# Optimization experiments

Hardware: AMD Instinct MI355X
Metric: run time of the kernel (lower is better)

The kernel has to match this reference:

```python
import jax, jax.numpy as jnp
import numpy as np

N, E = 50000, 800000
IN_DIM, H, OUT = 16, 256, 64
L = 3
REL_DIM, ROLE_DIM, COL_DIM = 16, 8, 8
NUM_REL, NUM_ROLE, NUM_COL = 8, 8, 3
EDGE_IN = 2 * H + REL_DIM + 2 * ROLE_DIM + 2 * COL_DIM   # 560
NODE_IN = 2 * H + ROLE_DIM + COL_DIM                     # 528
LN_EPS = 1e-5


def setup_inputs() -> dict:
    key = jax.random.key(0)
    ks = jax.random.split(key, 32)
    s = 0.02
    inp = {
        "scalars": jax.random.normal(ks[0], (N, IN_DIM), jnp.float32),
        "edge_index": jax.random.randint(ks[1], (2, E), 0, N),
        "edge_relation": jax.random.randint(ks[2], (E,), 0, NUM_REL),
        "node_color_rep": jax.random.randint(ks[3], (N,), 0, NUM_COL),
        "node_role": jax.random.randint(ks[4], (N,), 0, NUM_ROLE),
        # block-level embeddings + input projection (weights stored [in,out])
        "blk_role_emb": jax.random.normal(ks[5], (NUM_ROLE, 8), jnp.float32) * s,
        "blk_color_emb": jax.random.normal(ks[6], (NUM_COL, 8), jnp.float32) * s,
        "in_w": jax.random.normal(ks[7], (IN_DIM + 16, H), jnp.float32) * s,
        "in_b": jnp.zeros((H,), jnp.float32),
        # per-layer params, stacked over L
        "rel_embs": jax.random.normal(ks[8], (L, NUM_REL, REL_DIM), jnp.float32) * s,
        "role_embs": jax.random.normal(ks[9], (L, NUM_ROLE, ROLE_DIM), jnp.float32) * s,
        "col_embs": jax.random.normal(ks[10], (L, NUM_COL, COL_DIM), jnp.float32) * s,
        "e1_w": jax.random.normal(ks[11], (L, EDGE_IN, H), jnp.float32) * s,
        "e1_b": jnp.zeros((L, H), jnp.float32),
        "e2_w": jax.random.normal(ks[12], (L, H, H), jnp.float32) * s,
        "e2_b": jnp.zeros((L, H), jnp.float32),
        "n1_w": jax.random.normal(ks[13], (L, NODE_IN, H), jnp.float32) * s,
        "n1_b": jnp.zeros((L, H), jnp.float32),
        "n2_w": jax.random.normal(ks[14], (L, H, H), jnp.float32) * s,
        "n2_b": jnp.zeros((L, H), jnp.float32),
        "ln_g": jnp.ones((L, H), jnp.float32),
        "ln_b": jnp.zeros((L, H), jnp.float32),
        "out_w": jax.random.normal(ks[15], (H, OUT), jnp.float32) * s,
        "out_b": jnp.zeros((OUT,), jnp.float32),
    }
    return inp


def _layer(h, edge_index, edge_relation, node_color_rep, node_role,
           rel_e, role_e, col_e, e1w, e1b, e2w, e2b, n1w, n1b, n2w, n2b, g, b):
    src, dst = edge_index[0], edge_index[1]
    role_all = role_e[node_role]           # [N, ROLE_DIM]
    col_all = col_e[node_color_rep]        # [N, COL_DIM]
    edge_in = jnp.concatenate(
        [h[src], h[dst], rel_e[edge_relation],
         role_all[src], role_all[dst], col_all[src], col_all[dst]], axis=-1)
    m = jax.nn.silu(edge_in @ e1w + e1b)
    m = jax.nn.silu(m @ e2w + e2b)                       # [E, H]
    agg = jax.ops.segment_sum(m, dst, num_segments=h.shape[0])
    node_in = jnp.concatenate([h, agg, role_all, col_all], axis=-1)
    upd = jax.nn.silu(node_in @ n1w + n1b) @ n2w + n2b
    x = h + upd
    mu = jnp.mean(x, axis=-1, keepdims=True)
    var = jnp.mean(jnp.square(x - mu), axis=-1, keepdims=True)
    return g * (x - mu) * jax.lax.rsqrt(var + LN_EPS) + b


def reference(scalars, edge_index, edge_relation, node_color_rep, node_role,
              blk_role_emb, blk_color_emb, in_w, in_b,
              rel_embs, role_embs, col_embs,
              e1_w, e1_b, e2_w, e2_b, n1_w, n1_b, n2_w, n2_b,
              ln_g, ln_b, out_w, out_b):
    node_in = jnp.concatenate(
        [scalars, blk_color_emb[node_color_rep], blk_role_emb[node_role]], axis=-1)
    h = node_in @ in_w + in_b
    for i in range(L):
        h = _layer(h, edge_index, edge_relation, node_color_rep, node_role,
                   rel_embs[i], role_embs[i], col_embs[i],
                   e1_w[i], e1_b[i], e2_w[i], e2_b[i],
                   n1_w[i], n1_b[i], n2_w[i], n2_b[i],
                   ln_g[i], ln_b[i])
    return h @ out_w + out_b
```

## Files before the change

kernel.cpp:

```cpp
#include <hip/hip_runtime.h>

#define NN 50000
#define NE 800000
#define H 256
#define NB 12500
#define NBINS 50176
#define HBLK 782

typedef __bf16 bf16x8 __attribute__((ext_vector_type(8)));
typedef __bf16 bf16x4 __attribute__((ext_vector_type(4)));
typedef float f32x4 __attribute__((ext_vector_type(4)));

static __device__ __forceinline__ f32x4 mfma16(bf16x8 a, bf16x8 b, f32x4 c) {
  return __builtin_amdgcn_mfma_f32_16x16x32_bf16(a, b, c, 0, 0, 0);
}
static __device__ __forceinline__ bf16x8 bzero8() {
  bf16x8 z;
#pragma unroll
  for (int j = 0; j < 8; ++j) z[j] = (__bf16)0.f;
  return z;
}
static __device__ __forceinline__ float silu_f(float v) {
  return v * __builtin_amdgcn_rcpf(1.f + __builtin_amdgcn_exp2f(v * -1.442695041f));
}

__global__ void preph_kernel(
    const float* __restrict__ e1w, const float* __restrict__ e2w,
    const float* __restrict__ n1w, const float* __restrict__ n2w,
    const float* __restrict__ outw, const float* __restrict__ e1b,
    const float* __restrict__ n1b,
    const float* __restrict__ rel_embs, const float* __restrict__ role_embs,
    const float* __restrict__ col_embs, const int* __restrict__ dstI,
    __bf16* __restrict__ wsd, __bf16* __restrict__ e2p,
    __bf16* __restrict__ n1p, __bf16* __restrict__ n2p,
    __bf16* __restrict__ outp, int* __restrict__ cnt,
    float* __restrict__ TR, __bf16* __restrict__ TNp,
    __bf16* __restrict__ TSp, __bf16* __restrict__ TDp)
{
  if (blockIdx.x >= 4675) {
    const int e = (blockIdx.x - 4675) * 256 + threadIdx.x;
    if (e < NE) atomicAdd(&cnt[dstI[e]], 1);
    return;
  }
  int i = blockIdx.x * 256 + threadIdx.x;
  if (i < 3 * 131072) {
    const int l = i / 131072, rem = i % 131072;
    const int c = rem >> 14, r2 = rem & 16383;
    const int n = r2 >> 5, k = c * 32 + (r2 & 31);
    wsd[i] = (n < 256) ? (__bf16)e1w[((size_t)l * 560 + k) * 256 + n]
                       : (__bf16)e1w[((size_t)l * 560 + 256 + k) * 256 + (n - 256)];
    return;
  }
  i -= 3 * 131072;
  if (i < 3 * 65536) {
    const int l = i / 65536, rem = i % 65536;
    const int c = rem >> 13, r2 = rem & 8191;
    const int n = r2 >> 5, k = c * 32 + (r2 & 31);
    e2p[i] = (__bf16)e2w[((size_t)l * 256 + k) * 256 + n];
    return;
  }
  i -= 3 * 65536;
  if (i < 3 * 131072) {
    const int l = i / 131072, rem = i % 131072;
    const int c = rem >> 13, r2 = rem & 8191;
    const int n = r2 >> 5, k = c * 32 + (r2 & 31);
    n1p[i] = (__bf16)n1w[((size_t)l * 528 + k) * 256 + n];
    return;
  }
  i -= 3 * 131072;
  if (i < 3 * 65536) {
    const int l = i / 65536, rem = i % 65536;
    const int c = rem >> 13, r2 = rem & 8191;
    const int n = r2 >> 5, k = c * 32 + (r2 & 31);
    n2p[i] = (__bf16)n2w[((size_t)l * 256 + k) * 256 + n];
    return;
  }
  i -= 3 * 65536;
  if (i < 16384) {
    const int c = i >> 11, r2 = i & 2047;
    const int n = r2 >> 5, k = c * 32 + (r2 & 31);
    outp[i] = (__bf16)outw[(size_t)k * 64 + n];
    return;
  }
  i -= 16384;
  if (i < 768) {
    const int l = i >> 8, c = i & 255;
    float w[48];
#pragma unroll
    for (int j = 0; j < 48; ++j) w[j] = e1w[((size_t)l * 560 + 512 + j) * 256 + c];
#pragma unroll
    for (int r = 0; r < 8; ++r) {
      float s = 0.f;
#pragma unroll
      for (int j = 0; j < 16; ++j) s += rel_embs[l * 128 + r * 16 + j] * w[j];
      TR[((size_t)l * 8 + r) * 256 + c] = s;
    }
    float wn[16];
#pragma unroll
    for (int j = 0; j < 16; ++j) wn[j] = n1w[((size_t)l * 528 + 512 + j) * 256 + c];
    const float bias = e1b[l * 256 + c];
    const float nbias = n1b[l * 256 + c];
    const size_t ob = ((size_t)l * 256 + c) * 32;
#pragma unroll
    for (int ro = 0; ro < 8; ++ro) {
      float ss = 0.f, sd = 0.f, sn = 0.f;
#pragma unroll
      for (int j = 0; j < 8; ++j) {
        const float re = role_embs[l * 64 + ro * 8 + j];
        ss += re * w[16 + j];
        sd += re * w[24 + j];
        sn += re * wn[j];
      }
#pragma unroll
      for (int co = 0; co < 3; ++co) {
        float cs = 0.f, cd = 0.f, cn = 0.f;
#pragma unroll
        for (int j = 0; j < 8; ++j) {
          const float ce = col_embs[l * 24 + co * 8 + j];
          cs += ce * w[32 + j];
          cd += ce * w[40 + j];
          cn += ce * wn[8 + j];
        }
        const int k = ro * 3 + co;
        TSp[ob + k] = (__bf16)(ss + cs);
        TDp[ob + k] = (__bf16)(sd + cd + bias);
        TNp[ob + k] = (__bf16)(sn + cn + nbias);
      }
    }
#pragma unroll
    for (int k = 24; k < 32; ++k) {
      TSp[ob + k] = (__bf16)0.f;
      TDp[ob + k] = (__bf16)0.f;
      TNp[ob + k] = (__bf16)0.f;
    }
  }
}

__global__ __launch_bounds__(1024) void scan_kernel(int* __restrict__ cnt,
                                                    int* __restrict__ cnt2) {
  __shared__ int wsum[16];
  __shared__ int carry;
  const int tid = threadIdx.x, lane = tid & 63, wid = tid >> 6;
  if (tid == 0) carry = 0;
  __syncthreads();
  for (int base = 0; base < NBINS; base += 4096) {
    const int idx = base + tid * 4;
    int4 v = make_int4(0, 0, 0, 0);
    if (idx < NBINS) v = *(const int4*)&cnt[idx];
    const int s1 = v.x + v.y, s2 = s1 + v.z, tot = s2 + v.w;
    int x = tot;
#pragma unroll
    for (int d = 1; d < 64; d <<= 1) {
      const int y = __shfl_up(x, d, 64);
      if (lane >= d) x += y;
    }
    if (lane == 63) wsum[wid] = x;
    __syncthreads();
    int wpref = 0;
#pragma unroll
    for (int w = 0; w < 16; ++w)
      if (w < wid) wpref += wsum[w];
    const int ex = carry + wpref + (x - tot);
    if (idx < NBINS) {
      int4 o;
      o.x = ex; o.y = ex + v.x; o.z = ex + s1; o.w = ex + s2;
      *(int4*)&cnt[idx] = o;
      *(int4*)&cnt2[idx] = o;
    }
    __syncthreads();
    if (tid == 0) {
      int s = 0;
#pragma unroll
      for (int w = 0; w < 16; ++w) s += wsum[w];
      carry += s;
    }
    __syncthreads();
  }
}

__global__ void scat_kernel(const int* __restrict__ dstI, int* __restrict__ cnt,
                            const int* __restrict__ cnt2,
                            int* __restrict__ perm, int* __restrict__ dstS) {
  if (blockIdx.x >= 3125) {
    const int n = (blockIdx.x - 3125) * 256 + threadIdx.x;
    if (n < NN) {
      const int st = cnt2[n], en = cnt2[n + 1];
      for (int p = st; p < en; ++p) dstS[p] = n;
    }
    return;
  }
  const int e = blockIdx.x * 256 + threadIdx.x;
  if (e < NE) {
    const int pos = atomicAdd(&cnt[dstI[e]], 1);
    perm[pos] = e;
  }
}

__global__ __launch_bounds__(256, 2) void embed_kernel(
    const float* __restrict__ scalars, const int* __restrict__ ncol,
    const int* __restrict__ nrole,
    const float* __restrict__ colEmb, const float* __restrict__ roleEmb,
    const float* __restrict__ inw, const float* __restrict__ inb,
    const __bf16* __restrict__ wsd,
    const __bf16* __restrict__ TSp, const __bf16* __restrict__ TDp,
    __bf16* __restrict__ h, __bf16* __restrict__ PS, __bf16* __restrict__ PD)
{
  __shared__ __align__(16) char uni[37888];
  __shared__ int sTi[64];
  auto Ain = (__bf16 (*)[40])uni;
  auto Hs  = (__bf16 (*)[296])uni;

  const int tid  = threadIdx.x;
  const int lane = tid & 63;
  const int wave = tid >> 6;
  const int l15  = lane & 15;
  const int quad = lane >> 4;
  const int n0   = blockIdx.x * 64;
  const int colW = wave * 64;
  const int rowS = tid >> 5, colS = (tid & 31) * 8;

  if (tid < 64) {
    const int n = n0 + tid;
    sTi[tid] = (n < NN) ? (nrole[n] * 3 + ncol[n]) : 0;
  }
  {
    const int row = tid >> 2, q = tid & 3;
    const int n = n0 + row;
    __bf16* dp = &Ain[row][q * 8];
    if (n < NN) {
      if (q < 2) {
#pragma unroll
        for (int j = 0; j < 8; ++j) dp[j] = (__bf16)scalars[(size_t)n * 16 + q * 8 + j];
      } else if (q == 2) {
        const int c = ncol[n];
#pragma unroll
        for (int j = 0; j < 8; ++j) dp[j] = (__bf16)colEmb[c * 8 + j];
      } else {
        const int r = nrole[n];
#pragma unroll
        for (int j = 0; j < 8; ++j) dp[j] = (__bf16)roleEmb[r * 8 + j];
      }
    } else {
#pragma unroll
      for (int j = 0; j < 8; ++j) dp[j] = (__bf16)0.f;
    }
  }
  __syncthreads();

  f32x4 acc[4][4] = {};
  {
    bf16x8 bfr[4], afr[4];
#pragma unroll
    for (int nj = 0; nj < 4; ++nj) {
      const int col = colW + nj * 16 + l15;
#pragma unroll
      for (int j = 0; j < 8; ++j) bfr[nj][j] = (__bf16)inw[(quad * 8 + j) * 256 + col];
    }
#pragma unroll
    for (int mi = 0; mi < 4; ++mi)
      afr[mi] = *(const bf16x8*)&Ain[mi * 16 + l15][quad * 8];
#pragma unroll
    for (int mi = 0; mi < 4; ++mi)
#pragma unroll
      for (int nj = 0; nj < 4; ++nj)
        acc[mi][nj] = mfma16(afr[mi], bfr[nj], acc[mi][nj]);
  }
  float bi[4];
#pragma unroll
  for (int nj = 0; nj < 4; ++nj) bi[nj] = inb[colW + nj * 16 + l15];
  __syncthreads();

#pragma unroll
  for (int mi = 0; mi < 4; ++mi)
#pragma unroll
    for (int r = 0; r < 4; ++r) {
      const int row = mi * 16 + quad * 4 + r;
#pragma unroll
      for (int nj = 0; nj < 4; ++nj)
        Hs[row][colW + nj * 16 + l15] = (__bf16)(acc[mi][nj][r] + bi[nj]);
    }
  {
    const int row = tid >> 2, q = tid & 3;
    const int ti = sTi[row];
    bf16x8 v;
#pragma unroll
    for (int j = 0; j < 8; ++j) v[j] = (__bf16)((q * 8 + j == ti) ? 1.f : 0.f);
    *(bf16x8*)&Hs[row][256 + q * 8] = v;
  }
  __syncthreads();

#pragma unroll
  for (int it = 0; it < 8; ++it) {
    const int row = it * 8 + rowS;
    const int n = n0 + row;
    if (n < NN)
      *(bf16x8*)(h + (size_t)n * H + colS) = *(const bf16x8*)&Hs[row][colS];
  }

  f32x4 ap0[4][4] = {}, ap1[4][4] = {};
#pragma unroll
  for (int c = 0; c < 9; ++c) {
    bf16x8 afr[4];
#pragma unroll
    for (int mi = 0; mi < 4; ++mi)
      afr[mi] = *(const bf16x8*)&Hs[mi * 16 + l15][c * 32 + quad * 8];
    const __bf16* bp0 = (c < 8) ? wsd + ((size_t)c * 512) * 32 : TSp;
    const __bf16* bp1 = (c < 8) ? wsd + ((size_t)c * 512 + 256) * 32 : TDp;
#pragma unroll
    for (int nj = 0; nj < 4; ++nj) {
      const bf16x8 b0 = *(const bf16x8*)(bp0 + ((size_t)(colW + nj * 16 + l15)) * 32 + quad * 8);
      const bf16x8 b1 = *(const bf16x8*)(bp1 + ((size_t)(colW + nj * 16 + l15)) * 32 + quad * 8);
#pragma unroll
      for (int mi = 0; mi < 4; ++mi) {
        ap0[mi][nj] = mfma16(afr[mi], b0, ap0[mi][nj]);
        ap1[mi][nj] = mfma16(afr[mi], b1, ap1[mi][nj]);
      }
    }
  }
  __syncthreads();

#pragma unroll
  for (int hf = 0; hf < 2; ++hf) {
    if (hf) __syncthreads();
#pragma unroll
    for (int mi = 0; mi < 4; ++mi)
#pragma unroll
      for (int r = 0; r < 4; ++r) {
        const int row = mi * 16 + quad * 4 + r;
#pragma unroll
        for (int nj = 0; nj < 4; ++nj)
          Hs[row][colW + nj * 16 + l15] =
              (__bf16)(hf ? ap1[mi][nj][r] : ap0[mi][nj][r]);
      }
    __syncthreads();
    __bf16* P = hf ? PD : PS;
#pragma unroll
    for (int it = 0; it < 8; ++it) {
      const int row = it * 8 + rowS;
      const int n = n0 + row;
      if (n < NN)
        *(bf16x8*)(P + (size_t)n * H + colS) = *(const bf16x8*)&Hs[row][colS];
    }
  }
}

__global__ __launch_bounds__(256, 4) void edge_kernel(
    const __bf16* __restrict__ PS, const __bf16* __restrict__ PD,
    __bf16* __restrict__ agg, __bf16* __restrict__ bnd,
    const int* __restrict__ perm, const int* __restrict__ dstS,
    const int* __restrict__ srcI, const int* __restrict__ erel,
    const float* __restrict__ TR,
    const __bf16* __restrict__ e2p, const float* __restrict__ e2b)
{
  __shared__ __align__(16) char uni[34816];
  __shared__ __bf16 sTrel[8][256];
  __shared__ int sSrc[64], sDst[64], sRel[64];

  auto A2  = (__bf16 (*)[264])uni;
  auto A2t = (__bf16 (*)[68])uni;

  const int tid  = threadIdx.x;
  const int lane = tid & 63;
  const int wave = tid >> 6;
  const int l15  = lane & 15;
  const int quad = lane >> 4;
  const int e0   = blockIdx.x * 64;
  const int colW = wave * 64;

  if (tid < 64) {
    const int p = perm[e0 + tid];
    sSrc[tid] = srcI[p];
    sRel[tid] = erel[p];
    sDst[tid] = dstS[e0 + tid];
  }
  {
    const int r = tid >> 5, cs = (tid & 31) * 8;
    const float* p = TR + r * 256 + cs;
    bf16x8 v;
#pragma unroll
    for (int j = 0; j < 8; ++j) v[j] = (__bf16)p[j];
    *(bf16x8*)&sTrel[r][cs] = v;
  }
  __syncthreads();

  {
    const int brow = tid >> 5;
    const int cs = (tid & 31) * 8;
#pragma unroll
    for (int it = 0; it < 8; ++it) {
      const int row = it * 8 + brow;
      const bf16x8 a = *(const bf16x8*)(PS + (size_t)sSrc[row] * H + cs);
      const bf16x8 b = *(const bf16x8*)(PD + (size_t)sDst[row] * H + cs);
      const bf16x8 t = *(const bf16x8*)&sTrel[sRel[row]][cs];
      bf16x8 o;
#pragma unroll
      for (int j = 0; j < 8; ++j)
        o[j] = (__bf16)silu_f((float)a[j] + (float)b[j] + (float)t[j]);
      *(bf16x8*)&A2[row][cs] = o;
    }
  }
  __syncthreads();

  f32x4 acc2[4][4] = {};
#pragma unroll
  for (int c = 0; c < 8; ++c) {
    bf16x8 bfr[4], afr[4];
#pragma unroll
    for (int nj = 0; nj < 4; ++nj)
      bfr[nj] = *(const bf16x8*)(e2p + ((size_t)c * 256 + colW + nj * 16 + l15) * 32 + quad * 8);
#pragma unroll
    for (int mi = 0; mi < 4; ++mi)
      afr[mi] = *(const bf16x8*)&A2[mi * 16 + l15][c * 32 + quad * 8];
#pragma unroll
    for (int mi = 0; mi < 4; ++mi)
#pragma unroll
      for (int nj = 0; nj < 4; ++nj)
        acc2[mi][nj] = mfma16(afr[mi], bfr[nj], acc2[mi][nj]);
  }

  float b2[4];
#pragma unroll
  for (int nj = 0; nj < 4; ++nj) b2[nj] = e2b[colW + nj * 16 + l15];
  __syncthreads();

#pragma unroll
  for (int mi = 0; mi < 4; ++mi)
#pragma unroll
    for (int nj = 0; nj < 4; ++nj) {
      const int col = colW + nj * 16 + l15;
      bf16x4 pv;
#pragma unroll
      for (int r = 0; r < 4; ++r)
        pv[r] = (__bf16)silu_f(acc2[mi][nj][r] + b2[nj]);
      *(bf16x4*)&A2t[col][mi * 16 + quad * 4] = pv;
    }
  __syncthreads();

  {
    const int col = tid;
    const bool f = (lane > 0) && (sDst[lane] != sDst[lane - 1]);
    const unsigned long long mask = __ballot(f);
    bf16x4 v[16];
#pragma unroll
    for (int j = 0; j < 16; ++j) v[j] = *(const bf16x4*)&A2t[col][j * 4];
    __bf16* bnd0 = bnd + ((size_t)2 * blockIdx.x) * 256 + col;
    float sum = 0.f;
    int s0 = 0;
#pragma unroll
    for (int r = 0; r < 64; ++r) {
      sum += (float)v[r >> 2][r & 3];
      if (r == 63 || ((mask >> (r + 1)) & 1ull)) {
        const bool isFirst = (s0 == 0), isLast = (r == 63);
        if (isFirst) {
          bnd0[0] = (__bf16)(isLast ? 0.f : sum);
          if (isLast) bnd0[256] = (__bf16)sum;
        } else if (isLast) {
          bnd0[256] = (__bf16)sum;
        } else {
          agg[(size_t)sDst[r] * H + col] = (__bf16)sum;
        }
        sum = 0.f;
        s0 = r + 1;
      }
    }
  }
}

__global__ __launch_bounds__(256, 2) void node_kernel(
    __bf16* __restrict__ h, const __bf16* __restrict__ agg,
    const __bf16* __restrict__ bnd, const int* __restrict__ cnt2,
    const int* __restrict__ nrole, const int* __restrict__ ncol,
    const __bf16* __restrict__ n1p, const __bf16* __restrict__ TNp,
    const __bf16* __restrict__ n2p, const float* __restrict__ n2b,
    const float* __restrict__ lng, const float* __restrict__ lnb,
    const int mode,
    const __bf16* __restrict__ wsdN, const __bf16* __restrict__ TSpN,
    const __bf16* __restrict__ TDpN, __bf16* __restrict__ PS, __bf16* __restrict__ PD,
    const __bf16* __restrict__ outp, const float* __restrict__ outb,
    float* __restrict__ out)
{
  __shared__ __align__(16) char uni[37888];
  __shared__ float sSum[64][4], sSsq[64][4];
  __shared__ int sTi[64], sPcnt[64], sPidx[64][4];

  auto Abuf = (__bf16 (*)[72])uni;
  auto A2   = (__bf16 (*)[296])uni;

  const int tid  = threadIdx.x;
  const int lane = tid & 63;
  const int wave = tid >> 6;
  const int l15  = lane & 15;
  const int quad = lane >> 4;
  const int n0   = blockIdx.x * 64;
  const int colW = wave * 64;
  const int rowS = tid >> 5, colS = (tid & 31) * 8;

  if (tid < 64) {
    const int n = n0 + tid;
    int st = 0, en = 0, ti = 0;
    if (n < NN) {
      st = cnt2[n];
      en = cnt2[n + 1];
      ti = nrole[n] * 3 + ncol[n];
    }
    sTi[tid] = ti;
    int pc = 0, pidx[4] = {0, 0, 0, 0};
    if (en > st) {
      const int bs = st >> 6, be = (en - 1) >> 6;
      if (bs == be && (st & 63) != 0 && (en & 63) != 0) {
        pc = -1;
      } else {
        for (int b = bs; b <= be && pc < 4; ++b) {
          if (b > bs || (st & 63) == 0) pidx[pc++] = 2 * b;
          if ((b < be || (en & 63) == 0) && pc < 4) pidx[pc++] = 2 * b + 1;
        }
      }
    }
    sPcnt[tid] = pc;
#pragma unroll
    for (int j = 0; j < 4; ++j) sPidx[tid][j] = pidx[j];
  }
  __syncthreads();

  bf16x8 ibfr[2];
#pragma unroll
  for (int t = 0; t < 2; ++t)
#pragma unroll
    for (int j = 0; j < 8; ++j)
      ibfr[t][j] = (__bf16)((quad * 8 + j == t * 16 + l15) ? 1.f : 0.f);

  f32x4 acc[4][4] = {};
  f32x4 acch[4][4] = {};
  for (int s = 0; s < 8; ++s) {
    if (s) __syncthreads();
    if (s < 4) {
#pragma unroll
      for (int it = 0; it < 2; ++it) {
        const int t = tid + it * 256;
        const int row = t >> 3, seg = t & 7;
        const int n = n0 + row;
        bf16x8 v = bzero8();
        if (n < NN) v = *(const bf16x8*)(h + (size_t)n * H + s * 64 + seg * 8);
        *(bf16x8*)&Abuf[row][seg * 8] = v;
      }
    } else {
#pragma unroll
      for (int it = 0; it < 2; ++it) {
        const int t = tid + it * 256;
        const int row = t >> 3, seg = t & 7;
        const int off = (s - 4) * 64 + seg * 8;
        const int pc = sPcnt[row];
        bf16x8 v = bzero8();
        if (pc == -1) {
          v = *(const bf16x8*)(agg + (size_t)(n0 + row) * H + off);
        } else if (pc > 0) {
          float a8[8] = {0.f, 0.f, 0.f, 0.f, 0.f, 0.f, 0.f, 0.f};
          for (int j = 0; j < pc; ++j) {
            const bf16x8 pv = *(const bf16x8*)(bnd + (size_t)sPidx[row][j] * 256 + off);
#pragma unroll
            for (int k = 0; k < 8; ++k) a8[k] += (float)pv[k];
          }
#pragma unroll
          for (int k = 0; k < 8; ++k) v[k] = (__bf16)a8[k];
        }
        *(bf16x8*)&Abuf[row][seg * 8] = v;
      }
    }
    __syncthreads();
#pragma unroll
    for (int cc = 0; cc < 2; ++cc) {
      const int c = 2 * s + cc;
      bf16x8 bfr[4], afr[4];
#pragma unroll
      for (int nj = 0; nj < 4; ++nj)
        bfr[nj] = *(const bf16x8*)(n1p + ((size_t)c * 256 + colW + nj * 16 + l15) * 32 + quad * 8);
#pragma unroll
      for (int mi = 0; mi < 4; ++mi)
        afr[mi] = *(const bf16x8*)&Abuf[mi * 16 + l15][cc * 32 + quad * 8];
#pragma unroll
      for (int mi = 0; mi < 4; ++mi)
#pragma unroll
        for (int nj = 0; nj < 4; ++nj)
          acc[mi][nj] = mfma16(afr[mi], bfr[nj], acc[mi][nj]);
      if (s == wave) {
#pragma unroll
        for (int t = 0; t < 2; ++t)
#pragma unroll
          for (int mi = 0; mi < 4; ++mi)
            acch[mi][cc * 2 + t] = mfma16(afr[mi], ibfr[t], acch[mi][cc * 2 + t]);
      }
    }
  }
  __syncthreads();
  {
    const int row = tid >> 2, q = tid & 3;
    const int ti = sTi[row];
    bf16x8 v;
#pragma unroll
    for (int j = 0; j < 8; ++j) v[j] = (__bf16)((q * 8 + j == ti) ? 1.f : 0.f);
    *(bf16x8*)&Abuf[row][q * 8] = v;
  }
  __syncthreads();
  {
    bf16x8 bfr[4], afr[4];
#pragma unroll
    for (int nj = 0; nj < 4; ++nj)
      bfr[nj] = *(const bf16x8*)(TNp + ((size_t)(colW + nj * 16 + l15)) * 32 + quad * 8);
#pragma unroll
    for (int mi = 0; mi < 4; ++mi)
      afr[mi] = *(const bf16x8*)&Abuf[mi * 16 + l15][quad * 8];
#pragma unroll
    for (int mi = 0; mi < 4; ++mi)
#pragma unroll
      for (int nj = 0; nj < 4; ++nj)
        acc[mi][nj] = mfma16(afr[mi], bfr[nj], acc[mi][nj]);
  }
  __syncthreads();

#pragma unroll
  for (int mi = 0; mi < 4; ++mi)
#pragma unroll
    for (int r = 0; r < 4; ++r) {
      const int row = mi * 16 + quad * 4 + r;
#pragma unroll
      for (int nj = 0; nj < 4; ++nj)
        A2[row][colW + nj * 16 + l15] = (__bf16)silu_f(acc[mi][nj][r]);
    }
  __syncthreads();

  f32x4 acc2[4][4] = {};
#pragma unroll
  for (int c = 0; c < 8; ++c) {
    bf16x8 bfr[4], afr[4];
#pragma unroll
    for (int nj = 0; nj < 4; ++nj)
      bfr[nj] = *(const bf16x8*)(n2p + ((size_t)c * 256 + colW + nj * 16 + l15) * 32 + quad * 8);
#pragma unroll
    for (int mi = 0; mi < 4; ++mi)
      afr[mi] = *(const bf16x8*)&A2[mi * 16 + l15][c * 32 + quad * 8];
#pragma unroll
    for (int mi = 0; mi < 4; ++mi)
#pragma unroll
      for (int nj = 0; nj < 4; ++nj)
        acc2[mi][nj] = mfma16(afr[mi], bfr[nj], acc2[mi][nj]);
  }

  float b2[4], g4[4], bb4[4];
#pragma unroll
  for (int nj = 0; nj < 4; ++nj) {
    const int col = colW + nj * 16 + l15;
    b2[nj] = n2b[col]; g4[nj] = lng[col]; bb4[nj] = lnb[col];
  }
#pragma unroll
  for (int mi = 0; mi < 4; ++mi)
#pragma unroll
    for (int nj = 0; nj < 4; ++nj)
#pragma unroll
      for (int r = 0; r < 4; ++r)
        acc2[mi][nj][r] += b2[nj] + acch[mi][nj][r];

#pragma unroll
  for (int mi = 0; mi < 4; ++mi)
#pragma unroll
    for (int r = 0; r < 4; ++r) {
      float s1 = 0.f, s2 = 0.f;
#pragma unroll
      for (int nj = 0; nj < 4; ++nj) {
        const float v = acc2[mi][nj][r];
        s1 += v; s2 += v * v;
      }
#pragma unroll
      for (int d = 1; d < 16; d <<= 1) {
        s1 += __shfl_xor(s1, d, 16);
        s2 += __shfl_xor(s2, d, 16);
      }
      if (l15 == 0) {
        const int row = mi * 16 + quad * 4 + r;
        sSum[row][wave] = s1; sSsq[row][wave] = s2;
      }
    }
  __syncthreads();

#pragma unroll
  for (int mi = 0; mi < 4; ++mi)
#pragma unroll
    for (int r = 0; r < 4; ++r) {
      const int row = mi * 16 + quad * 4 + r;
      const float t1 = sSum[row][0] + sSum[row][1] + sSum[row][2] + sSum[row][3];
      const float t2 = sSsq[row][0] + sSsq[row][1] + sSsq[row][2] + sSsq[row][3];
      const float mu = t1 * (1.f / 256.f);
      float var = t2 * (1.f / 256.f) - mu * mu;
      var = var < 0.f ? 0.f : var;
      const float rstd = rsqrtf(var + 1e-5f);
#pragma unroll
      for (int nj = 0; nj < 4; ++nj) {
        const int col = colW + nj * 16 + l15;
        const float o = g4[nj] * (acc2[mi][nj][r] - mu) * rstd + bb4[nj];
        A2[row][col] = (__bf16)o;
      }
    }
  if (mode == 0) {
    const int row = tid >> 2, q = tid & 3;
    const int ti = sTi[row];
    bf16x8 v;
#pragma unroll
    for (int j = 0; j < 8; ++j) v[j] = (__bf16)((q * 8 + j == ti) ? 1.f : 0.f);
    *(bf16x8*)&A2[row][256 + q * 8] = v;
  }
  __syncthreads();

  if (mode == 0) {
#pragma unroll
    for (int it = 0; it < 8; ++it) {
      const int row = it * 8 + rowS;
      const int n = n0 + row;
      if (n < NN)
        *(bf16x8*)(h + (size_t)n * H + colS) = *(const bf16x8*)&A2[row][colS];
    }
    f32x4 ap0[4][4] = {}, ap1[4][4] = {};
#pragma unroll
    for (int c = 0; c < 9; ++c) {
      bf16x8 afr[4];
#pragma unroll
      for (int mi = 0; mi < 4; ++mi)
        afr[mi] = *(const bf16x8*)&A2[mi * 16 + l15][c * 32 + quad * 8];
      const __bf16* bp0 = (c < 8) ? wsdN + ((size_t)c * 512) * 32 : TSpN;
      const __bf16* bp1 = (c < 8) ? wsdN + ((size_t)c * 512 + 256) * 32 : TDpN;
#pragma unroll
      for (int nj = 0; nj < 4; ++nj) {
        const bf16x8 b0 = *(const bf16x8*)(bp0 + ((size_t)(colW + nj * 16 + l15)) * 32 + quad * 8);
        const bf16x8 b1 = *(const bf16x8*)(bp1 + ((size_t)(colW + nj * 16 + l15)) * 32 + quad * 8);
#pragma unroll
        for (int mi = 0; mi < 4; ++mi) {
          ap0[mi][nj] = mfma16(afr[mi], b0, ap0[mi][nj]);
          ap1[mi][nj] = mfma16(afr[mi], b1, ap1[mi][nj]);
        }
      }
    }
    __syncthreads();
#pragma unroll
    for (int hf = 0; hf < 2; ++hf) {
      if (hf) __syncthreads();
#pragma unroll
      for (int mi = 0; mi < 4; ++mi)
#pragma unroll
        for (int r = 0; r < 4; ++r) {
          const int row = mi * 16 + quad * 4 + r;
#pragma unroll
          for (int nj = 0; nj < 4; ++nj)
            A2[row][colW + nj * 16 + l15] =
                (__bf16)(hf ? ap1[mi][nj][r] : ap0[mi][nj][r]);
        }
      __syncthreads();
      __bf16* P = hf ? PD : PS;
#pragma unroll
      for (int it = 0; it < 8; ++it) {
        const int row = it * 8 + rowS;
        const int n = n0 + row;
        if (n < NN)
          *(bf16x8*)(P + (size_t)n * H + colS) = *(const bf16x8*)&A2[row][colS];
      }
    }
  } else {
    f32x4 ao[4] = {};
#pragma unroll
    for (int c = 0; c < 8; ++c) {
      const bf16x8 bfr = *(const bf16x8*)(outp + ((size_t)c * 64 + wave * 16 + l15) * 32 + quad * 8);
#pragma unroll
      for (int mi = 0; mi < 4; ++mi) {
        const bf16x8 afr = *(const bf16x8*)&A2[mi * 16 + l15][c * 32 + quad * 8];
        ao[mi] = mfma16(afr, bfr, ao[mi]);
      }
    }
    const float ob = outb[wave * 16 + l15];
#pragma unroll
    for (int mi = 0; mi < 4; ++mi)
#pragma unroll
      for (int r = 0; r < 4; ++r) {
        const int n = n0 + mi * 16 + quad * 4 + r;
        if (n < NN) out[(size_t)n * 64 + wave * 16 + l15] = ao[mi][r] + ob;
      }
  }
}

extern "C" void kernel_launch(void* const* d_in, const int* in_sizes, int n_in,
                              void* d_out, int out_size, void* d_ws, size_t ws_size,
                              hipStream_t stream) {
  const float* scalars   = (const float*)d_in[0];
  const int*   ei        = (const int*)d_in[1];
  const int*   erel      = (const int*)d_in[2];
  const int*   ncol      = (const int*)d_in[3];
  const int*   nrole     = (const int*)d_in[4];
  const float* blk_role  = (const float*)d_in[5];
  const float* blk_col   = (const float*)d_in[6];
  const float* inw       = (const float*)d_in[7];
  const float* inb       = (const float*)d_in[8];
  const float* rel_embs  = (const float*)d_in[9];
  const float* role_embs = (const float*)d_in[10];
  const float* col_embs  = (const float*)d_in[11];
  const float* e1w       = (const float*)d_in[12];
  const float* e1b       = (const float*)d_in[13];
  const float* e2w       = (const float*)d_in[14];
  const float* e2b       = (const float*)d_in[15];
  const float* n1w       = (const float*)d_in[16];
  const float* n1b       = (const float*)d_in[17];
  const float* n2w       = (const float*)d_in[18];
  const float* n2b       = (const float*)d_in[19];
  const float* lng       = (const float*)d_in[20];
  const float* lnb       = (const float*)d_in[21];
  const float* outw      = (const float*)d_in[22];
  const float* outb      = (const float*)d_in[23];

  const int* srcI = ei;
  const int* dstI = ei + NE;

  char* ws = (char*)d_ws;
  size_t off = 0;
  auto take = [&](size_t bytes) -> char* {
    off = (off + 255) & ~(size_t)255;
    char* p = ws + off;
    off += bytes;
    return p;
  };
  __bf16* h    = (__bf16*)take((size_t)NN * H * 2);
  __bf16* agg  = (__bf16*)take((size_t)NN * H * 2);
  __bf16* bnd  = (__bf16*)take((size_t)2 * NB * 256 * 2);
  __bf16* PS   = (__bf16*)take((size_t)NN * H * 2);
  __bf16* PD   = (__bf16*)take((size_t)NN * H * 2);
  __bf16* wsd  = (__bf16*)take((size_t)3 * 131072 * 2);
  __bf16* e2p  = (__bf16*)take((size_t)3 * 65536 * 2);
  __bf16* n1p  = (__bf16*)take((size_t)3 * 131072 * 2);
  __bf16* n2p  = (__bf16*)take((size_t)3 * 65536 * 2);
  __bf16* outp = (__bf16*)take((size_t)16384 * 2);
  float*  TR   = (float*)take((size_t)3 * 8 * 256 * 4);
  __bf16* TNp  = (__bf16*)take((size_t)3 * 8192 * 2);
  __bf16* TSp  = (__bf16*)take((size_t)3 * 8192 * 2);
  __bf16* TDp  = (__bf16*)take((size_t)3 * 8192 * 2);
  int*    cnt  = (int*)take((size_t)NBINS * 4);
  int*    cnt2 = (int*)take((size_t)NBINS * 4);
  int*    perm = (int*)take((size_t)NE * 4);
  int*    dstS = (int*)take((size_t)NE * 4);

  hipMemsetAsync(cnt, 0, (size_t)NBINS * 4, stream);
  preph_kernel<<<7800, 256, 0, stream>>>(
      e1w, e2w, n1w, n2w, outw, e1b, n1b, rel_embs, role_embs, col_embs, dstI,
      wsd, e2p, n1p, n2p, outp, cnt, TR, TNp, TSp, TDp);
  scan_kernel<<<1, 1024, 0, stream>>>(cnt, cnt2);
  scat_kernel<<<3321, 256, 0, stream>>>(dstI, cnt, cnt2, perm, dstS);
  embed_kernel<<<HBLK, 256, 0, stream>>>(
      scalars, ncol, nrole, blk_col, blk_role, inw, inb,
      wsd, TSp, TDp, h, PS, PD);

  for (int l = 0; l < 3; ++l) {
    edge_kernel<<<NB, 256, 0, stream>>>(
        PS, PD, agg, bnd, perm, dstS, srcI, erel, TR + (size_t)l * 2048,
        e2p + (size_t)l * 65536, e2b + (size_t)l * 256);
    const int mode = (l < 2) ? 0 : 1;
    const int ln = (l + 1 < 3) ? l + 1 : 0;
    node_kernel<<<HBLK, 256, 0, stream>>>(
        h, agg, bnd, cnt2, nrole, ncol,
        n1p + (size_t)l * 131072, TNp + (size_t)l * 8192,
        n2p + (size_t)l * 65536,  n2b + (size_t)l * 256,
        lng + (size_t)l * 256, lnb + (size_t)l * 256,
        mode,
        wsd + (size_t)ln * 131072, TSp + (size_t)ln * 8192, TDp + (size_t)ln * 8192,
        PS, PD, outp, outb, (float*)d_out);
  }
}
```

Before: 1.169 ms.

## Split next-layer edge projection into separate kernel and pack edge src/rel

Moves the per-node PS/PD projection for the next layer out of node_kernel and embed_kernel into a new pre_kernel. It launches two blocks per 64-node group, one for each half, so each block holds fewer accumulators. This lowers register and LDS pressure, letting node_kernel run at occupancy 4 and dropping the identity-MFMA residual trick in favour of re-reading h. The scatter step now stores src and relation packed into one int in sorted order, which removes the perm indirection in edge_kernel. The relation table is stored in bf16. The cost is extra kernel launches and an extra read of h per layer.

```diff
diff --git a/kernel.cpp b/kernel.cpp
--- a/kernel.cpp
+++ b/kernel.cpp
@@ -34,7 +34,7 @@
     __bf16* __restrict__ wsd, __bf16* __restrict__ e2p,
     __bf16* __restrict__ n1p, __bf16* __restrict__ n2p,
     __bf16* __restrict__ outp, int* __restrict__ cnt,
-    float* __restrict__ TR, __bf16* __restrict__ TNp,
+    __bf16* __restrict__ TRb, __bf16* __restrict__ TNp,
     __bf16* __restrict__ TSp, __bf16* __restrict__ TDp)
 {
   if (blockIdx.x >= 4675) {
@@ -93,7 +93,7 @@
       float s = 0.f;
 #pragma unroll
       for (int j = 0; j < 16; ++j) s += rel_embs[l * 128 + r * 16 + j] * w[j];
-      TR[((size_t)l * 8 + r) * 256 + c] = s;
+      TRb[((size_t)l * 8 + r) * 256 + c] = (__bf16)s;
     }
     float wn[16];
 #pragma unroll
@@ -178,10 +178,26 @@
   }
 }
 
-__global__ void scat_kernel(const int* __restrict__ dstI, int* __restrict__ cnt,
-                            const int* __restrict__ cnt2,
-                            int* __restrict__ perm, int* __restrict__ dstS) {
-  if (blockIdx.x >= 3125) {
+__global__ __launch_bounds__(256, 4) void scem_kernel(
+    const int* __restrict__ srcI, const int* __restrict__ dstI,
+    const int* __restrict__ erel, int* __restrict__ cnt,
+    const int* __restrict__ cnt2,
+    int* __restrict__ esr, int* __restrict__ dstS,
+    const float* __restrict__ scalars, const int* __restrict__ ncol,
+    const int* __restrict__ nrole,
+    const float* __restrict__ colEmb, const float* __restrict__ roleEmb,
+    const float* __restrict__ inw, const float* __restrict__ inb,
+    __bf16* __restrict__ h)
+{
+  if (blockIdx.x < 3125) {
+    const int e = blockIdx.x * 256 + threadIdx.x;
+    if (e < NE) {
+      const int pos = atomicAdd(&cnt[dstI[e]], 1);
+      esr[pos] = srcI[e] | (erel[e] << 16);
+    }
+    return;
+  }
+  if (blockIdx.x < 3321) {
     const int n = (blockIdx.x - 3125) * 256 + threadIdx.x;
     if (n < NN) {
       const int st = cnt2[n], en = cnt2[n + 1];
@@ -189,40 +205,19 @@
     }
     return;
   }
-  const int e = blockIdx.x * 256 + threadIdx.x;
-  if (e < NE) {
-    const int pos = atomicAdd(&cnt[dstI[e]], 1);
-    perm[pos] = e;
-  }
-}
-
-__global__ __launch_bounds__(256, 2) void embed_kernel(
-    const float* __restrict__ scalars, const int* __restrict__ ncol,
-    const int* __restrict__ nrole,
-    const float* __restrict__ colEmb, const float* __restrict__ roleEmb,
-    const float* __restrict__ inw, const float* __restrict__ inb,
-    const __bf16* __restrict__ wsd,
-    const __bf16* __restrict__ TSp, const __bf16* __restrict__ TDp,
-    __bf16* __restrict__ h, __bf16* __restrict__ PS, __bf16* __restrict__ PD)
-{
-  __shared__ __align__(16) char uni[37888];
-  __shared__ int sTi[64];
+  __shared__ __align__(16) char uni[33792];
   auto Ain = (__bf16 (*)[40])uni;
-  auto Hs  = (__bf16 (*)[296])uni;
+  auto Hs  = (__bf16 (*)[264])uni;
 
   const int tid  = threadIdx.x;
   const int lane = tid & 63;
   const int wave = tid >> 6;
   const int l15  = lane & 15;
   const int quad = lane >> 4;
-  const int n0   = blockIdx.x * 64;
+  const int n0   = (blockIdx.x - 3321) * 64;
   const int colW = wave * 64;
   const int rowS = tid >> 5, colS = (tid & 31) * 8;
 
-  if (tid < 64) {
-    const int n = n0 + tid;
-    sTi[tid] = (n < NN) ? (nrole[n] * 3 + ncol[n]) : 0;
-  }
   {
     const int row = tid >> 2, q = tid & 3;
     const int n = n0 + row;
@@ -279,16 +274,7 @@
       for (int nj = 0; nj < 4; ++nj)
         Hs[row][colW + nj * 16 + l15] = (__bf16)(acc[mi][nj][r] + bi[nj]);
     }
-  {
-    const int row = tid >> 2, q = tid & 3;
-    const int ti = sTi[row];
-    bf16x8 v;
-#pragma unroll
-    for (int j = 0; j < 8; ++j) v[j] = (__bf16)((q * 8 + j == ti) ? 1.f : 0.f);
-    *(bf16x8*)&Hs[row][256 + q * 8] = v;
-  }
-  __syncthreads();
-
+  __syncthreads();
 #pragma unroll
   for (int it = 0; it < 8; ++it) {
     const int row = it * 8 + rowS;
@@ -296,60 +282,96 @@
     if (n < NN)
       *(bf16x8*)(h + (size_t)n * H + colS) = *(const bf16x8*)&Hs[row][colS];
   }
-
-  f32x4 ap0[4][4] = {}, ap1[4][4] = {};
+}
+
+__global__ __launch_bounds__(256, 4) void pre_kernel(
+    const __bf16* __restrict__ h, const int* __restrict__ nrole,
+    const int* __restrict__ ncol, const __bf16* __restrict__ wsd,
+    const __bf16* __restrict__ TSp, const __bf16* __restrict__ TDp,
+    __bf16* __restrict__ PS, __bf16* __restrict__ PD)
+{
+  __shared__ __align__(16) __bf16 Hs[64][296];
+  __shared__ int sTi[64];
+
+  const int tid  = threadIdx.x;
+  const int lane = tid & 63;
+  const int wave = tid >> 6;
+  const int l15  = lane & 15;
+  const int quad = lane >> 4;
+  const int ng   = blockIdx.x >> 1;
+  const int hf   = blockIdx.x & 1;
+  const int n0   = ng * 64;
+  const int colW = wave * 64;
+  const int rowS = tid >> 5, colS = (tid & 31) * 8;
+
+  if (tid < 64) {
+    const int n = n0 + tid;
+    sTi[tid] = (n < NN) ? (nrole[n] * 3 + ncol[n]) : 0;
+  }
+#pragma unroll
+  for (int it = 0; it < 8; ++it) {
+    const int row = it * 8 + rowS;
+    const int n = n0 + row;
+    bf16x8 v = bzero8();
+    if (n < NN) v = *(const bf16x8*)(h + (size_t)n * H + colS);
+    *(bf16x8*)&Hs[row][colS] = v;
+  }
+  __syncthreads();
+  {
+    const int row = tid >> 2, q = tid & 3;
+    const int ti = sTi[row];
+    bf16x8 v;
+#pragma unroll
+    for (int j = 0; j < 8; ++j) v[j] = (__bf16)((q * 8 + j == ti) ? 1.f : 0.f);
+    *(bf16x8*)&Hs[row][256 + q * 8] = v;
+  }
+  __syncthreads();
+
+  f32x4 ap[4][4] = {};
 #pragma unroll
   for (int c = 0; c < 9; ++c) {
-    bf16x8 afr[4];
+    const __bf16* bp = (c < 8) ? wsd + ((size_t)c * 512 + hf * 256) * 32
+                               : (hf ? TDp : TSp);
+    bf16x8 bfr[4], afr[4];
+#pragma unroll
+    for (int nj = 0; nj < 4; ++nj)
+      bfr[nj] = *(const bf16x8*)(bp + ((size_t)(colW + nj * 16 + l15)) * 32 + quad * 8);
 #pragma unroll
     for (int mi = 0; mi < 4; ++mi)
       afr[mi] = *(const bf16x8*)&Hs[mi * 16 + l15][c * 32 + quad * 8];
-    const __bf16* bp0 = (c < 8) ? wsd + ((size_t)c * 512) * 32 : TSp;
-    const __bf16* bp1 = (c < 8) ? wsd + ((size_t)c * 512 + 256) * 32 : TDp;
-#pragma unroll
-    for (int nj = 0; nj < 4; ++nj) {
-      const bf16x8 b0 = *(const bf16x8*)(bp0 + ((size_t)(colW + nj * 16 + l15)) * 32 + quad * 8);
-      const bf16x8 b1 = *(const bf16x8*)(bp1 + ((size_t)(colW + nj * 16 + l15)) * 32 + quad * 8);
-#pragma unroll
-      for (int mi = 0; mi < 4; ++mi) {
-        ap0[mi][nj] = mfma16(afr[mi], b0, ap0[mi][nj]);
-        ap1[mi][nj] = mfma16(afr[mi], b1, ap1[mi][nj]);
-      }
-    }
-  }
-  __syncthreads();
-
-#pragma unroll
-  for (int hf = 0; hf < 2; ++hf) {
-    if (hf) __syncthreads();
-#pragma unroll
-    for (int mi = 0; mi < 4; ++mi)
-#pragma unroll
-      for (int r = 0; r < 4; ++r) {
-        const int row = mi * 16 + quad * 4 + r;
-#pragma unroll
-        for (int nj = 0; nj < 4; ++nj)
-          Hs[row][colW + nj * 16 + l15] =
-              (__bf16)(hf ? ap1[mi][nj][r] : ap0[mi][nj][r]);
-      }
-    __syncthreads();
-    __bf16* P = hf ? PD : PS;
-#pragma unroll
-    for (int it = 0; it < 8; ++it) {
-      const int row = it * 8 + rowS;
-      const int n = n0 + row;
-      if (n < NN)
-        *(bf16x8*)(P + (size_t)n * H + colS) = *(const bf16x8*)&Hs[row][colS];
-    }
+#pragma unroll
+    for (int mi = 0; mi < 4; ++mi)
+#pragma unroll
+      for (int nj = 0; nj < 4; ++nj)
+        ap[mi][nj] = mfma16(afr[mi], bfr[nj], ap[mi][nj]);
+  }
+  __syncthreads();
+
+#pragma unroll
+  for (int mi = 0; mi < 4; ++mi)
+#pragma unroll
+    for (int r = 0; r < 4; ++r) {
+      const int row = mi * 16 + quad * 4 + r;
+#pragma unroll
+      for (int nj = 0; nj < 4; ++nj)
+        Hs[row][colW + nj * 16 + l15] = (__bf16)ap[mi][nj][r];
+    }
+  __syncthreads();
+  __bf16* P = hf ? PD : PS;
+#pragma unroll
+  for (int it = 0; it < 8; ++it) {
+    const int row = it * 8 + rowS;
+    const int n = n0 + row;
+    if (n < NN)
+      *(bf16x8*)(P + (size_t)n * H + colS) = *(const bf16x8*)&Hs[row][colS];
   }
 }
 
 __global__ __launch_bounds__(256, 4) void edge_kernel(
     const __bf16* __restrict__ PS, const __bf16* __restrict__ PD,
     __bf16* __restrict__ agg, __bf16* __restrict__ bnd,
-    const int* __restrict__ perm, const int* __restrict__ dstS,
-    const int* __restrict__ srcI, const int* __restrict__ erel,
-    const float* __restrict__ TR,
+    const int* __restrict__ esr, const int* __restrict__ dstS,
+    const __bf16* __restrict__ TRb,
     const __bf16* __restrict__ e2p, const float* __restrict__ e2b)
 {
   __shared__ __align__(16) char uni[34816];
@@ -368,18 +390,14 @@
   const int colW = wave * 64;
 
   if (tid < 64) {
-    const int p = perm[e0 + tid];
-    sSrc[tid] = srcI[p];
-    sRel[tid] = erel[p];
+    const int u = esr[e0 + tid];
+    sSrc[tid] = u & 0xffff;
+    sRel[tid] = u >> 16;
     sDst[tid] = dstS[e0 + tid];
   }
   {
     const int r = tid >> 5, cs = (tid & 31) * 8;
-    const float* p = TR + r * 256 + cs;
-    bf16x8 v;
-#pragma unroll
-    for (int j = 0; j < 8; ++j) v[j] = (__bf16)p[j];
-    *(bf16x8*)&sTrel[r][cs] = v;
+    *(bf16x8*)&sTrel[r][cs] = *(const bf16x8*)(TRb + r * 256 + cs);
   }
   __syncthreads();
 
@@ -466,7 +484,7 @@
   }
 }
 
-__global__ __launch_bounds__(256, 2) void node_kernel(
+__global__ __launch_bounds__(256, 4) void node_kernel(
     __bf16* __restrict__ h, const __bf16* __restrict__ agg,
     const __bf16* __restrict__ bnd, const int* __restrict__ cnt2,
     const int* __restrict__ nrole, const int* __restrict__ ncol,
@@ -474,17 +492,15 @@
     const __bf16* __restrict__ n2p, const float* __restrict__ n2b,
     const float* __restrict__ lng, const float* __restrict__ lnb,
     const int mode,
-    const __bf16* __restrict__ wsdN, const __bf16* __restrict__ TSpN,
-    const __bf16* __restrict__ TDpN, __bf16* __restrict__ PS, __bf16* __restrict__ PD,
     const __bf16* __restrict__ outp, const float* __restrict__ outb,
     float* __restrict__ out)
 {
-  __shared__ __align__(16) char uni[37888];
+  __shared__ __align__(16) char uni[33792];
   __shared__ float sSum[64][4], sSsq[64][4];
   __shared__ int sTi[64], sPcnt[64], sPidx[64][4];
 
   auto Abuf = (__bf16 (*)[72])uni;
-  auto A2   = (__bf16 (*)[296])uni;
+  auto A2   = (__bf16 (*)[264])uni;
 
   const int tid  = threadIdx.x;
   const int lane = tid & 63;
@@ -522,15 +538,7 @@
   }
   __syncthreads();
 
-  bf16x8 ibfr[2];
-#pragma unroll
-  for (int t = 0; t < 2; ++t)
-#pragma unroll
-    for (int j = 0; j < 8; ++j)
-      ibfr[t][j] = (__bf16)((quad * 8 + j == t * 16 + l15) ? 1.f : 0.f);
-
   f32x4 acc[4][4] = {};
-  f32x4 acch[4][4] = {};
   for (int s = 0; s < 8; ++s) {
     if (s) __syncthreads();
     if (s < 4) {
@@ -582,13 +590,6 @@
 #pragma unroll
         for (int nj = 0; nj < 4; ++nj)
           acc[mi][nj] = mfma16(afr[mi], bfr[nj], acc[mi][nj]);
-      if (s == wave) {
-#pragma unroll
-        for (int t = 0; t < 2; ++t)
-#pragma unroll
-          for (int mi = 0; mi < 4; ++mi)
-            acch[mi][cc * 2 + t] = mfma16(afr[mi], ibfr[t], acch[mi][cc * 2 + t]);
-      }
     }
   }
   __syncthreads();
@@ -644,6 +645,17 @@
       for (int nj = 0; nj < 4; ++nj)
         acc2[mi][nj] = mfma16(afr[mi], bfr[nj], acc2[mi][nj]);
   }
+  __syncthreads();
+
+#pragma unroll
+  for (int it = 0; it < 8; ++it) {
+    const int row = it * 8 + rowS;
+    const int n = n0 + row;
+    bf16x8 v = bzero8();
+    if (n < NN) v = *(const bf16x8*)(h + (size_t)n * H + colS);
+    *(bf16x8*)&A2[row][colS] = v;
+  }
+  __syncthreads();
 
   float b2[4], g4[4], bb4[4];
 #pragma unroll
@@ -654,10 +666,12 @@
 #pragma unroll
   for (int mi = 0; mi < 4; ++mi)
 #pragma unroll
-    for (int nj = 0; nj < 4; ++nj)
+    for (int nj = 0; nj < 4; ++nj) {
+      const int col = colW + nj * 16 + l15;
 #pragma unroll
       for (int r = 0; r < 4; ++r)
-        acc2[mi][nj][r] += b2[nj] + acch[mi][nj][r];
+        acc2[mi][nj][r] += b2[nj] + (float)A2[mi * 16 + quad * 4 + r][col];
+    }
 
 #pragma unroll
   for (int mi = 0; mi < 4; ++mi)
@@ -699,14 +713,6 @@
         A2[row][col] = (__bf16)o;
       }
     }
-  if (mode == 0) {
-    const int row = tid >> 2, q = tid & 3;
-    const int ti = sTi[row];
-    bf16x8 v;
-#pragma unroll
-    for (int j = 0; j < 8; ++j) v[j] = (__bf16)((q * 8 + j == ti) ? 1.f : 0.f);
-    *(bf16x8*)&A2[row][256 + q * 8] = v;
-  }
   __syncthreads();
 
   if (mode == 0) {
@@ -716,50 +722,6 @@
       const int n = n0 + row;
       if (n < NN)
         *(bf16x8*)(h + (size_t)n * H + colS) = *(const bf16x8*)&A2[row][colS];
-    }
-    f32x4 ap0[4][4] = {}, ap1[4][4] = {};
-#pragma unroll
-    for (int c = 0; c < 9; ++c) {
-      bf16x8 afr[4];
-#pragma unroll
-      for (int mi = 0; mi < 4; ++mi)
-        afr[mi] = *(const bf16x8*)&A2[mi * 16 + l15][c * 32 + quad * 8];
-      const __bf16* bp0 = (c < 8) ? wsdN + ((size_t)c * 512) * 32 : TSpN;
-      const __bf16* bp1 = (c < 8) ? wsdN + ((size_t)c * 512 + 256) * 32 : TDpN;
-#pragma unroll
-      for (int nj = 0; nj < 4; ++nj) {
-        const bf16x8 b0 = *(const bf16x8*)(bp0 + ((size_t)(colW + nj * 16 + l15)) * 32 + quad * 8);
-        const bf16x8 b1 = *(const bf16x8*)(bp1 + ((size_t)(colW + nj * 16 + l15)) * 32 + quad * 8);
-#pragma unroll
-        for (int mi = 0; mi < 4; ++mi) {
-          ap0[mi][nj] = mfma16(afr[mi], b0, ap0[mi][nj]);
-          ap1[mi][nj] = mfma16(afr[mi], b1, ap1[mi][nj]);
-        }
-      }
-    }
-    __syncthreads();
-#pragma unroll
-    for (int hf = 0; hf < 2; ++hf) {
-      if (hf) __syncthreads();
-#pragma unroll
-      for (int mi = 0; mi < 4; ++mi)
-#pragma unroll
-        for (int r = 0; r < 4; ++r) {
-          const int row = mi * 16 + quad * 4 + r;
-#pragma unroll
-          for (int nj = 0; nj < 4; ++nj)
-            A2[row][colW + nj * 16 + l15] =
-                (__bf16)(hf ? ap1[mi][nj][r] : ap0[mi][nj][r]);
-        }
-      __syncthreads();
-      __bf16* P = hf ? PD : PS;
-#pragma unroll
-      for (int it = 0; it < 8; ++it) {
-        const int row = it * 8 + rowS;
-        const int n = n0 + row;
-        if (n < NN)
-          *(bf16x8*)(P + (size_t)n * H + colS) = *(const bf16x8*)&A2[row][colS];
-      }
     }
   } else {
     f32x4 ao[4] = {};
@@ -832,38 +794,42 @@
   __bf16* n1p  = (__bf16*)take((size_t)3 * 131072 * 2);
   __bf16* n2p  = (__bf16*)take((size_t)3 * 65536 * 2);
   __bf16* outp = (__bf16*)take((size_t)16384 * 2);
-  float*  TR   = (float*)take((size_t)3 * 8 * 256 * 4);
+  __bf16* TRb  = (__bf16*)take((size_t)3 * 8 * 256 * 2);
   __bf16* TNp  = (__bf16*)take((size_t)3 * 8192 * 2);
   __bf16* TSp  = (__bf16*)take((size_t)3 * 8192 * 2);
   __bf16* TDp  = (__bf16*)take((size_t)3 * 8192 * 2);
   int*    cnt  = (int*)take((size_t)NBINS * 4);
   int*    cnt2 = (int*)take((size_t)NBINS * 4);
-  int*    perm = (int*)take((size_t)NE * 4);
+  int*    esr  = (int*)take((size_t)NE * 4);
   int*    dstS = (int*)take((size_t)NE * 4);
 
   hipMemsetAsync(cnt, 0, (size_t)NBINS * 4, stream);
   preph_kernel<<<7800, 256, 0, stream>>>(
       e1w, e2w, n1w, n2w, outw, e1b, n1b, rel_embs, role_embs, col_embs, dstI,
-      wsd, e2p, n1p, n2p, outp, cnt, TR, TNp, TSp, TDp);
+      wsd, e2p, n1p, n2p, outp, cnt, TRb, TNp, TSp, TDp);
   scan_kernel<<<1, 1024, 0, stream>>>(cnt, cnt2);
-  scat_kernel<<<3321, 256, 0, stream>>>(dstI, cnt, cnt2, perm, dstS);
-  embed_kernel<<<HBLK, 256, 0, stream>>>(
-      scalars, ncol, nrole, blk_col, blk_role, inw, inb,
-      wsd, TSp, TDp, h, PS, PD);
+  scem_kernel<<<4103, 256, 0, stream>>>(
+      srcI, dstI, erel, cnt, cnt2, esr, dstS,
+      scalars, ncol, nrole, blk_col, blk_role, inw, inb, h);
+  pre_kernel<<<2 * HBLK, 256, 0, stream>>>(
+      h, nrole, ncol, wsd, TSp, TDp, PS, PD);
 
   for (int l = 0; l < 3; ++l) {
     edge_kernel<<<NB, 256, 0, stream>>>(
-        PS, PD, agg, bnd, perm, dstS, srcI, erel, TR + (size_t)l * 2048,
+        PS, PD, agg, bnd, esr, dstS, TRb + (size_t)l * 2048,
         e2p + (size_t)l * 65536, e2b + (size_t)l * 256);
     const int mode = (l < 2) ? 0 : 1;
-    const int ln = (l + 1 < 3) ? l + 1 : 0;
     node_kernel<<<HBLK, 256, 0, stream>>>(
         h, agg, bnd, cnt2, nrole, ncol,
         n1p + (size_t)l * 131072, TNp + (size_t)l * 8192,
         n2p + (size_t)l * 65536,  n2b + (size_t)l * 256,
         lng + (size_t)l * 256, lnb + (size_t)l * 256,
-        mode,
-        wsd + (size_t)ln * 131072, TSp + (size_t)ln * 8192, TDp + (size_t)ln * 8192,
-        PS, PD, outp, outb, (float*)d_out);
-  }
-}
+        mode, outp, outb, (float*)d_out);
+    if (l < 2) {
+      const int ln = l + 1;
+      pre_kernel<<<2 * HBLK, 256, 0, stream>>>(
+          h, nrole, ncol, wsd + (size_t)ln * 131072,
+          TSp + (size_t)ln * 8192, TDp + (size_t)ln * 8192, PS, PD);
+    }
+  }
+}
```

Measured after the change: 1.148 ms. Within noise of the previous version (-1.8%).
